# Kernel tuning notes

Hardware: AMD Instinct MI355X
Metric: run time of the kernel (lower is better)

The kernel has to match this reference:

```python
import jax, jax.numpy as jnp
import numpy as np

N_NODES = 100000
N_EDGES = 300000
F = 256


def setup_inputs() -> dict:
    key = jax.random.key(0)
    k1, k2, k3, k4, k5, k6 = jax.random.split(key, 6)
    x = jax.random.normal(k1, (N_NODES, F), dtype=jnp.float32)
    edge_index = jax.random.randint(k2, (2, N_EDGES), 0, N_NODES, dtype=jnp.int32)
    # GCNConv learned params (PyG: lin weight [out,in] applied as x @ W.T; store as [in,out])
    W_conv = jax.random.normal(k3, (F, F), dtype=jnp.float32) / np.sqrt(F)
    b_conv = jax.random.normal(k4, (F,), dtype=jnp.float32) * 0.01
    W_lin = jax.random.normal(k5, (F, 1), dtype=jnp.float32) / np.sqrt(F)
    b_lin = jax.random.normal(k6, (1,), dtype=jnp.float32) * 0.01
    return {"x": x, "edge_index": edge_index, "W_conv": W_conv,
            "b_conv": b_conv, "W_lin": W_lin, "b_lin": b_lin}


def gcn_conv(x, edge_index, W_conv, b_conv):
    N = x.shape[0]
    # add self loops (PyG default add_self_loops=True)
    loop = jnp.arange(N, dtype=edge_index.dtype)
    src = jnp.concatenate([edge_index[0], loop])
    dst = jnp.concatenate([edge_index[1], loop])
    # symmetric normalization: deg over destination, norm = d^-1/2[src]*d^-1/2[dst]
    deg = jax.ops.segment_sum(jnp.ones_like(dst, dtype=x.dtype), dst, num_segments=N)
    dinv = jnp.where(deg > 0, jax.lax.rsqrt(deg), 0.0)
    norm = dinv[src] * dinv[dst]  # [E+N]
    h = x @ W_conv  # [N,F] dense transform first (PyG order)
    msg = h[src] * norm[:, None]  # gather + scale, [E+N, F]
    agg = jax.ops.segment_sum(msg, dst, num_segments=N)  # scatter-add, [N,F]
    return agg + b_conv


def reference(x, edge_index, W_conv, b_conv, W_lin, b_lin):
    h = jax.nn.relu(gcn_conv(x, edge_index, W_conv, b_conv))
    return jax.nn.sigmoid(h @ W_lin + b_lin)  # [N,1]
```

## Files before the change

kernel.cpp:

```cpp
#include <hip/hip_runtime.h>
#include <hip/hip_bf16.h>
#include <math.h>

#define FDIM 256

typedef short bfrag __attribute__((ext_vector_type(8)));
typedef short s16x4 __attribute__((ext_vector_type(4)));
typedef float f32x4 __attribute__((ext_vector_type(4)));
typedef unsigned short u16x8 __attribute__((ext_vector_type(8)));

__device__ __forceinline__ short f2bf_rne(float f) {
    uint32_t u = __float_as_uint(f);
    uint32_t r = (u + 0x7FFFu + ((u >> 16) & 1u)) >> 16;
    return (short)r;
}
__device__ __forceinline__ float bf2f(unsigned short s) {
    return __uint_as_float(((uint32_t)s) << 16);
}

#define GLOAD_LDS16(g, l) __builtin_amdgcn_global_load_lds(              \
    (const __attribute__((address_space(1))) void*)(g),                  \
    (__attribute__((address_space(3))) void*)(l), 16, 0, 0)

__global__ void count_kernel(const int* __restrict__ dst, int* __restrict__ counts, int E) {
    int e = blockIdx.x * 256 + threadIdx.x;
    if (e < E) atomicAdd(&counts[dst[e]], 1);
}

__global__ void scan1_kernel(const int* __restrict__ counts, int* __restrict__ blksums, int N) {
    __shared__ int sd[256];
    int tid = threadIdx.x;
    int base = blockIdx.x * 1024 + tid * 4;
    int s = 0;
#pragma unroll
    for (int t = 0; t < 4; ++t) { int i = base + t; if (i < N) s += counts[i]; }
    sd[tid] = s; __syncthreads();
    for (int off = 128; off > 0; off >>= 1) {
        if (tid < off) sd[tid] += sd[tid + off];
        __syncthreads();
    }
    if (tid == 0) blksums[blockIdx.x] = sd[0];
}

__global__ void scan2_kernel(int* __restrict__ blksums, int NB) {
    __shared__ int sd[128];
    int tid = threadIdx.x;
    int v = (tid < NB) ? blksums[tid] : 0;
    sd[tid] = v; __syncthreads();
    for (int off = 1; off < 128; off <<= 1) {
        int t = (tid >= off) ? sd[tid - off] : 0;
        __syncthreads();
        sd[tid] += t;
        __syncthreads();
    }
    if (tid < NB) blksums[tid] = sd[tid] - v;
}

__global__ void scan3_kernel(const int* __restrict__ counts, const int* __restrict__ blksums,
                             int* __restrict__ offsets, int* __restrict__ cursor,
                             float* __restrict__ dinv, int N, int E) {
    __shared__ int sd[256];
    int tid = threadIdx.x;
    int base = blockIdx.x * 1024 + tid * 4;
    int c[4]; int s = 0;
#pragma unroll
    for (int t = 0; t < 4; ++t) { int i = base + t; c[t] = (i < N) ? counts[i] : 0; s += c[t]; }
    sd[tid] = s; __syncthreads();
    int v = s;
    for (int off = 1; off < 256; off <<= 1) {
        int t = (tid >= off) ? sd[tid - off] : 0;
        __syncthreads();
        sd[tid] += t;
        __syncthreads();
    }
    int run = sd[tid] - v + blksums[blockIdx.x];
#pragma unroll
    for (int t = 0; t < 4; ++t) {
        int i = base + t;
        if (i < N) {
            offsets[i] = run;
            cursor[i]  = run;
            dinv[i] = rsqrtf((float)(c[t] + 1));
            run += c[t];
        }
    }
    if (blockIdx.x == 0 && tid == 0) offsets[N] = E;
}

__global__ void fill_kernel(const int* __restrict__ src, const int* __restrict__ dst,
                            int* __restrict__ cursor, int* __restrict__ csr_src, int E) {
    int e = blockIdx.x * 256 + threadIdx.x;
    if (e < E) {
        int s = src[e], d = dst[e];
        int pos = atomicAdd(&cursor[d], 1);
        csr_src[pos] = s;
    }
}

__global__ void wsplit_kernel(const float* __restrict__ W,
                              short* __restrict__ Wh, short* __restrict__ Wl) {
    const int k = blockIdx.x;
    const int n = threadIdx.x;
    const float w = W[k * 256 + n];
    const short hi = f2bf_rne(w);
    const short lo = f2bf_rne(w - bf2f((unsigned short)hi));
    const int s = k >> 5, g = (k & 31) >> 3, j = k & 7;
    const size_t idx = (size_t)s * 8192 + n * 32 + g * 8 + j;
    Wh[idx] = hi; Wl[idx] = lo;
}

__global__ __launch_bounds__(512, 4) void gemm_mfma(const float* __restrict__ X,
                                                    const short* __restrict__ Wth,
                                                    const short* __restrict__ Wtl,
                                                    const float* __restrict__ dinv,
                                                    unsigned short* __restrict__ Hb, int N) {
    __shared__ short Xh[2][2048], Xl[2][2048];
    __shared__ short Wh[2][8192], Wl[2][8192];

    const int tid  = threadIdx.x;
    const int lane = tid & 63;
    const int wid  = tid >> 6;
    const int wm   = wid >> 2;
    const int wn   = wid & 3;
    const int row0 = blockIdx.x * 64;
    const int g    = lane >> 4;
    const int r15  = lane & 15;

    const int srow = tid >> 3, skq = tid & 7;
    const int sg = skq >> 1, sj = (skq & 1) * 4;
    const int xoff = (srow * 4 + sg) * 8 + sj;
    const int xrow = row0 + srow;
    const float* xptr = X + (size_t)xrow * FDIM + skq * 4;

    f32x4 acc[2][4];
#pragma unroll
    for (int i = 0; i < 2; ++i)
#pragma unroll
        for (int j = 0; j < 4; ++j) acc[i][j] = (f32x4){0.f, 0.f, 0.f, 0.f};

    float4 xa;
    xa = (xrow < N) ? *(const float4*)xptr : make_float4(0, 0, 0, 0);
    {
        const float v[4] = {xa.x, xa.y, xa.z, xa.w};
        s16x4 hi4, lo4;
#pragma unroll
        for (int j = 0; j < 4; ++j) {
            const short h = f2bf_rne(v[j]);
            hi4[j] = h; lo4[j] = f2bf_rne(v[j] - bf2f((unsigned short)h));
        }
        *(s16x4*)(&Xh[0][xoff]) = hi4;
        *(s16x4*)(&Xl[0][xoff]) = lo4;
    }
#pragma unroll
    for (int p = 0; p < 2; ++p) {
        GLOAD_LDS16(Wth + p * 4096 + tid * 8, &Wh[0][p * 4096 + tid * 8]);
        GLOAD_LDS16(Wtl + p * 4096 + tid * 8, &Wl[0][p * 4096 + tid * 8]);
    }
    xa = (xrow < N) ? *(const float4*)(xptr + 32) : make_float4(0, 0, 0, 0);
    __syncthreads();

    for (int s = 0; s < 8; ++s) {
        const int cur = s & 1, nxt = cur ^ 1;
        if (s < 7) {
            const float v[4] = {xa.x, xa.y, xa.z, xa.w};
            s16x4 hi4, lo4;
#pragma unroll
            for (int j = 0; j < 4; ++j) {
                const short h = f2bf_rne(v[j]);
                hi4[j] = h; lo4[j] = f2bf_rne(v[j] - bf2f((unsigned short)h));
            }
            *(s16x4*)(&Xh[nxt][xoff]) = hi4;
            *(s16x4*)(&Xl[nxt][xoff]) = lo4;
            const short* gh = Wth + (s + 1) * 8192;
            const short* gl = Wtl + (s + 1) * 8192;
#pragma unroll
            for (int p = 0; p < 2; ++p) {
                GLOAD_LDS16(gh + p * 4096 + tid * 8, &Wh[nxt][p * 4096 + tid * 8]);
                GLOAD_LDS16(gl + p * 4096 + tid * 8, &Wl[nxt][p * 4096 + tid * 8]);
            }
        }
        if (s < 6)
            xa = (xrow < N) ? *(const float4*)(xptr + (s + 2) * 32) : make_float4(0, 0, 0, 0);

        bfrag ah[2], al[2], bh[4], bl[4];
#pragma unroll
        for (int mi = 0; mi < 2; ++mi) {
            const int off = ((wm * 32 + mi * 16 + r15) * 4 + g) * 8;
            ah[mi] = *(const bfrag*)(&Xh[cur][off]);
            al[mi] = *(const bfrag*)(&Xl[cur][off]);
        }
#pragma unroll
        for (int ni = 0; ni < 4; ++ni) {
            const int off = ((wn * 64 + ni * 16 + r15) * 4 + g) * 8;
            bh[ni] = *(const bfrag*)(&Wh[cur][off]);
            bl[ni] = *(const bfrag*)(&Wl[cur][off]);
        }
#pragma unroll
        for (int mi = 0; mi < 2; ++mi)
#pragma unroll
            for (int ni = 0; ni < 4; ++ni)
                acc[mi][ni] = __builtin_amdgcn_mfma_f32_16x16x32_bf16(ah[mi], bh[ni], acc[mi][ni], 0, 0, 0);
#pragma unroll
        for (int mi = 0; mi < 2; ++mi)
#pragma unroll
            for (int ni = 0; ni < 4; ++ni)
                acc[mi][ni] = __builtin_amdgcn_mfma_f32_16x16x32_bf16(ah[mi], bl[ni], acc[mi][ni], 0, 0, 0);
#pragma unroll
        for (int mi = 0; mi < 2; ++mi)
#pragma unroll
            for (int ni = 0; ni < 4; ++ni)
                acc[mi][ni] = __builtin_amdgcn_mfma_f32_16x16x32_bf16(al[mi], bh[ni], acc[mi][ni], 0, 0, 0);

        if (s < 7) __syncthreads();
    }

#pragma unroll
    for (int mi = 0; mi < 2; ++mi) {
        const int rowb = row0 + wm * 32 + mi * 16 + g * 4;
#pragma unroll
        for (int r = 0; r < 4; ++r) {
            const int row = rowb + r;
            if (row < N) {
                const float dv = dinv[row];
                unsigned short* base = Hb + (size_t)row * FDIM + wn * 64 + r15;
#pragma unroll
                for (int ni = 0; ni < 4; ++ni)
                    base[ni * 16] = (unsigned short)f2bf_rne(acc[mi][ni][r] * dv);
            }
        }
    }
}

__global__ __launch_bounds__(256) void agg_kernel(const unsigned short* __restrict__ hb,
                                                  const int* __restrict__ offsets,
                                                  const int* __restrict__ csr_src,
                                                  const float* __restrict__ dinv,
                                                  const float* __restrict__ b_conv,
                                                  const float* __restrict__ W_lin,
                                                  const float* __restrict__ b_lin,
                                                  float* __restrict__ out, int N) {
    const int t    = threadIdx.x;
    const int l16  = t & 15;
    const int node = blockIdx.x * 16 + (t >> 4);
    if (node >= N) return;

    const int start = offsets[node];
    const int end   = offsets[node + 1];

    float acc[16];
    {
        const unsigned short* r = hb + (size_t)node * FDIM + l16 * 16;
        const u16x8 u0 = *(const u16x8*)r, u1 = *(const u16x8*)(r + 8);
#pragma unroll
        for (int k = 0; k < 8; ++k) { acc[k] = bf2f(u0[k]); acc[8 + k] = bf2f(u1[k]); }
    }
    for (int j = start; j < end; ++j) {
        const unsigned short* r = hb + (size_t)csr_src[j] * FDIM + l16 * 16;
        const u16x8 u0 = *(const u16x8*)r, u1 = *(const u16x8*)(r + 8);
#pragma unroll
        for (int k = 0; k < 8; ++k) { acc[k] += bf2f(u0[k]); acc[8 + k] += bf2f(u1[k]); }
    }

    const float dv = dinv[node];
    float p = 0.f;
#pragma unroll
    for (int q = 0; q < 4; ++q) {
        const float4 bc = *(const float4*)(b_conv + l16 * 16 + q * 4);
        const float4 wl = *(const float4*)(W_lin  + l16 * 16 + q * 4);
        p = fmaf(fmaxf(fmaf(acc[q * 4 + 0], dv, bc.x), 0.f), wl.x, p);
        p = fmaf(fmaxf(fmaf(acc[q * 4 + 1], dv, bc.y), 0.f), wl.y, p);
        p = fmaf(fmaxf(fmaf(acc[q * 4 + 2], dv, bc.z), 0.f), wl.z, p);
        p = fmaf(fmaxf(fmaf(acc[q * 4 + 3], dv, bc.w), 0.f), wl.w, p);
    }
#pragma unroll
    for (int off = 1; off < 16; off <<= 1) p += __shfl_xor(p, off);
    if (l16 == 0) out[node] = 1.f / (1.f + expf(-(p + b_lin[0])));
}

extern "C" void kernel_launch(void* const* d_in, const int* in_sizes, int n_in,
                              void* d_out, int out_size, void* d_ws, size_t ws_size,
                              hipStream_t stream) {
    const float* x      = (const float*)d_in[0];
    const int*   eidx   = (const int*)d_in[1];
    const float* W_conv = (const float*)d_in[2];
    const float* b_conv = (const float*)d_in[3];
    const float* W_lin  = (const float*)d_in[4];
    const float* b_lin  = (const float*)d_in[5];
    float* out = (float*)d_out;

    const int N = in_sizes[0] / FDIM;
    const int E = in_sizes[1] / 2;
    const int* e_src = eidx;
    const int* e_dst = eidx + E;

    char* p = (char*)d_ws;
    unsigned short* hb = (unsigned short*)p; p += (size_t)N * FDIM * sizeof(unsigned short);
    int* counts   = (int*)p;        p += (size_t)N * sizeof(int);
    int* offsets  = (int*)p;        p += (size_t)(N + 1) * sizeof(int);
    int* cursor   = (int*)p;        p += (size_t)N * sizeof(int);
    float* dinv   = (float*)p;      p += (size_t)N * sizeof(float);
    int* csr_src  = (int*)p;        p += (size_t)E * sizeof(int);
    int* blksums  = (int*)p;        p += 128 * sizeof(int);
    short* Wth    = (short*)p;      p += (size_t)FDIM * FDIM * sizeof(short);
    short* Wtl    = (short*)p;      p += (size_t)FDIM * FDIM * sizeof(short);

    const int NB = (N + 1023) / 1024;

    hipMemsetAsync(counts, 0, (size_t)N * sizeof(int), stream);

    count_kernel<<<(E + 255) / 256, 256, 0, stream>>>(e_dst, counts, E);
    scan1_kernel<<<NB, 256, 0, stream>>>(counts, blksums, N);
    scan2_kernel<<<1, 128, 0, stream>>>(blksums, NB);
    scan3_kernel<<<NB, 256, 0, stream>>>(counts, blksums, offsets, cursor, dinv, N, E);
    fill_kernel<<<(E + 255) / 256, 256, 0, stream>>>(e_src, e_dst, cursor, csr_src, E);

    wsplit_kernel<<<FDIM, FDIM, 0, stream>>>(W_conv, Wth, Wtl);

    gemm_mfma<<<(N + 63) / 64, 512, 0, stream>>>(x, Wth, Wtl, dinv, hb, N);

    agg_kernel<<<(N + 15) / 16, 256, 0, stream>>>(hb, offsets, csr_src, dinv,
                                                  b_conv, W_lin, b_lin, out, N);
}
```

Measured before the change: 269.2 us.

## Load W fragments directly to registers in GEMM and unroll edge gather by two

The GEMM no longer stages the split-bf16 W tiles through LDS with global_load_lds. Each wave now loads its B fragments straight from global memory (cache-resident) into double-buffered registers one k-step ahead. The X LDS tile is relaid out as k-group-major to change its bank access pattern, and the k-loop is fully unrolled. The aggregation kernel processes two neighbours per iteration with two accumulator sets to expose more memory-level parallelism, at the cost of more registers, which may reduce occupancy.

```diff
diff --git a/kernel.cpp b/kernel.cpp
--- a/kernel.cpp
+++ b/kernel.cpp
@@ -17,10 +17,6 @@
 __device__ __forceinline__ float bf2f(unsigned short s) {
     return __uint_as_float(((uint32_t)s) << 16);
 }
-
-#define GLOAD_LDS16(g, l) __builtin_amdgcn_global_load_lds(              \
-    (const __attribute__((address_space(1))) void*)(g),                  \
-    (__attribute__((address_space(3))) void*)(l), 16, 0, 0)
 
 __global__ void count_kernel(const int* __restrict__ dst, int* __restrict__ counts, int E) {
     int e = blockIdx.x * 256 + threadIdx.x;
@@ -115,7 +111,6 @@
                                                     const float* __restrict__ dinv,
                                                     unsigned short* __restrict__ Hb, int N) {
     __shared__ short Xh[2][2048], Xl[2][2048];
-    __shared__ short Wh[2][8192], Wl[2][8192];
 
     const int tid  = threadIdx.x;
     const int lane = tid & 63;
@@ -126,9 +121,11 @@
     const int g    = lane >> 4;
     const int r15  = lane & 15;
 
+    const short* WhP = Wth + (wn * 64 + r15) * 32 + g * 8;
+    const short* WlP = Wtl + (wn * 64 + r15) * 32 + g * 8;
+
     const int srow = tid >> 3, skq = tid & 7;
-    const int sg = skq >> 1, sj = (skq & 1) * 4;
-    const int xoff = (srow * 4 + sg) * 8 + sj;
+    const int xsidx = (skq >> 1) * 512 + srow * 8 + (skq & 1) * 4;
     const int xrow = row0 + srow;
     const float* xptr = X + (size_t)xrow * FDIM + skq * 4;
 
@@ -138,8 +135,9 @@
 #pragma unroll
         for (int j = 0; j < 4; ++j) acc[i][j] = (f32x4){0.f, 0.f, 0.f, 0.f};
 
-    float4 xa;
-    xa = (xrow < N) ? *(const float4*)xptr : make_float4(0, 0, 0, 0);
+    bfrag bh[2][4], bl[2][4];
+
+    float4 xa = (xrow < N) ? *(const float4*)xptr : make_float4(0, 0, 0, 0);
     {
         const float v[4] = {xa.x, xa.y, xa.z, xa.w};
         s16x4 hi4, lo4;
@@ -148,19 +146,21 @@
             const short h = f2bf_rne(v[j]);
             hi4[j] = h; lo4[j] = f2bf_rne(v[j] - bf2f((unsigned short)h));
         }
-        *(s16x4*)(&Xh[0][xoff]) = hi4;
-        *(s16x4*)(&Xl[0][xoff]) = lo4;
-    }
-#pragma unroll
-    for (int p = 0; p < 2; ++p) {
-        GLOAD_LDS16(Wth + p * 4096 + tid * 8, &Wh[0][p * 4096 + tid * 8]);
-        GLOAD_LDS16(Wtl + p * 4096 + tid * 8, &Wl[0][p * 4096 + tid * 8]);
+        *(s16x4*)(&Xh[0][xsidx]) = hi4;
+        *(s16x4*)(&Xl[0][xsidx]) = lo4;
+    }
+#pragma unroll
+    for (int ni = 0; ni < 4; ++ni) {
+        bh[0][ni] = *(const bfrag*)(WhP + ni * 512);
+        bl[0][ni] = *(const bfrag*)(WlP + ni * 512);
     }
     xa = (xrow < N) ? *(const float4*)(xptr + 32) : make_float4(0, 0, 0, 0);
     __syncthreads();
 
+#pragma unroll
     for (int s = 0; s < 8; ++s) {
         const int cur = s & 1, nxt = cur ^ 1;
+
         if (s < 7) {
             const float v[4] = {xa.x, xa.y, xa.z, xa.w};
             s16x4 hi4, lo4;
@@ -169,47 +169,43 @@
                 const short h = f2bf_rne(v[j]);
                 hi4[j] = h; lo4[j] = f2bf_rne(v[j] - bf2f((unsigned short)h));
             }
-            *(s16x4*)(&Xh[nxt][xoff]) = hi4;
-            *(s16x4*)(&Xl[nxt][xoff]) = lo4;
-            const short* gh = Wth + (s + 1) * 8192;
-            const short* gl = Wtl + (s + 1) * 8192;
-#pragma unroll
-            for (int p = 0; p < 2; ++p) {
-                GLOAD_LDS16(gh + p * 4096 + tid * 8, &Wh[nxt][p * 4096 + tid * 8]);
-                GLOAD_LDS16(gl + p * 4096 + tid * 8, &Wl[nxt][p * 4096 + tid * 8]);
-            }
+            *(s16x4*)(&Xh[nxt][xsidx]) = hi4;
+            *(s16x4*)(&Xl[nxt][xsidx]) = lo4;
         }
         if (s < 6)
             xa = (xrow < N) ? *(const float4*)(xptr + (s + 2) * 32) : make_float4(0, 0, 0, 0);
 
-        bfrag ah[2], al[2], bh[4], bl[4];
+        if (s < 7) {
+#pragma unroll
+            for (int ni = 0; ni < 4; ++ni) {
+                bh[nxt][ni] = *(const bfrag*)(WhP + (s + 1) * 8192 + ni * 512);
+                bl[nxt][ni] = *(const bfrag*)(WlP + (s + 1) * 8192 + ni * 512);
+            }
+        }
+
+        bfrag ah[2], al[2];
 #pragma unroll
         for (int mi = 0; mi < 2; ++mi) {
-            const int off = ((wm * 32 + mi * 16 + r15) * 4 + g) * 8;
+            const int off = g * 512 + (wm * 32 + mi * 16 + r15) * 8;
             ah[mi] = *(const bfrag*)(&Xh[cur][off]);
             al[mi] = *(const bfrag*)(&Xl[cur][off]);
         }
-#pragma unroll
-        for (int ni = 0; ni < 4; ++ni) {
-            const int off = ((wn * 64 + ni * 16 + r15) * 4 + g) * 8;
-            bh[ni] = *(const bfrag*)(&Wh[cur][off]);
-            bl[ni] = *(const bfrag*)(&Wl[cur][off]);
-        }
+
 #pragma unroll
         for (int mi = 0; mi < 2; ++mi)
 #pragma unroll
             for (int ni = 0; ni < 4; ++ni)
-                acc[mi][ni] = __builtin_amdgcn_mfma_f32_16x16x32_bf16(ah[mi], bh[ni], acc[mi][ni], 0, 0, 0);
+                acc[mi][ni] = __builtin_amdgcn_mfma_f32_16x16x32_bf16(ah[mi], bh[cur][ni], acc[mi][ni], 0, 0, 0);
 #pragma unroll
         for (int mi = 0; mi < 2; ++mi)
 #pragma unroll
             for (int ni = 0; ni < 4; ++ni)
-                acc[mi][ni] = __builtin_amdgcn_mfma_f32_16x16x32_bf16(ah[mi], bl[ni], acc[mi][ni], 0, 0, 0);
+                acc[mi][ni] = __builtin_amdgcn_mfma_f32_16x16x32_bf16(ah[mi], bl[cur][ni], acc[mi][ni], 0, 0, 0);
 #pragma unroll
         for (int mi = 0; mi < 2; ++mi)
 #pragma unroll
             for (int ni = 0; ni < 4; ++ni)
-                acc[mi][ni] = __builtin_amdgcn_mfma_f32_16x16x32_bf16(al[mi], bh[ni], acc[mi][ni], 0, 0, 0);
+                acc[mi][ni] = __builtin_amdgcn_mfma_f32_16x16x32_bf16(al[mi], bh[cur][ni], acc[mi][ni], 0, 0, 0);
 
         if (s < 7) __syncthreads();
     }
@@ -247,18 +243,33 @@
     const int start = offsets[node];
     const int end   = offsets[node + 1];
 
-    float acc[16];
+    float accA[16], accB[16];
     {
         const unsigned short* r = hb + (size_t)node * FDIM + l16 * 16;
         const u16x8 u0 = *(const u16x8*)r, u1 = *(const u16x8*)(r + 8);
 #pragma unroll
-        for (int k = 0; k < 8; ++k) { acc[k] = bf2f(u0[k]); acc[8 + k] = bf2f(u1[k]); }
-    }
-    for (int j = start; j < end; ++j) {
-        const unsigned short* r = hb + (size_t)csr_src[j] * FDIM + l16 * 16;
-        const u16x8 u0 = *(const u16x8*)r, u1 = *(const u16x8*)(r + 8);
-#pragma unroll
-        for (int k = 0; k < 8; ++k) { acc[k] += bf2f(u0[k]); acc[8 + k] += bf2f(u1[k]); }
+        for (int k = 0; k < 8; ++k) {
+            accA[k] = bf2f(u0[k]); accA[8 + k] = bf2f(u1[k]);
+            accB[k] = 0.f;         accB[8 + k] = 0.f;
+        }
+    }
+    int j = start;
+    for (; j + 1 < end; j += 2) {
+        const unsigned short* ra = hb + (size_t)csr_src[j]     * FDIM + l16 * 16;
+        const unsigned short* rb = hb + (size_t)csr_src[j + 1] * FDIM + l16 * 16;
+        const u16x8 a0 = *(const u16x8*)ra, a1 = *(const u16x8*)(ra + 8);
+        const u16x8 b0 = *(const u16x8*)rb, b1 = *(const u16x8*)(rb + 8);
+#pragma unroll
+        for (int k = 0; k < 8; ++k) {
+            accA[k] += bf2f(a0[k]); accA[8 + k] += bf2f(a1[k]);
+            accB[k] += bf2f(b0[k]); accB[8 + k] += bf2f(b1[k]);
+        }
+    }
+    if (j < end) {
+        const unsigned short* ra = hb + (size_t)csr_src[j] * FDIM + l16 * 16;
+        const u16x8 a0 = *(const u16x8*)ra, a1 = *(const u16x8*)(ra + 8);
+#pragma unroll
+        for (int k = 0; k < 8; ++k) { accA[k] += bf2f(a0[k]); accA[8 + k] += bf2f(a1[k]); }
     }
 
     const float dv = dinv[node];
@@ -267,10 +278,10 @@
     for (int q = 0; q < 4; ++q) {
         const float4 bc = *(const float4*)(b_conv + l16 * 16 + q * 4);
         const float4 wl = *(const float4*)(W_lin  + l16 * 16 + q * 4);
-        p = fmaf(fmaxf(fmaf(acc[q * 4 + 0], dv, bc.x), 0.f), wl.x, p);
-        p = fmaf(fmaxf(fmaf(acc[q * 4 + 1], dv, bc.y), 0.f), wl.y, p);
-        p = fmaf(fmaxf(fmaf(acc[q * 4 + 2], dv, bc.z), 0.f), wl.z, p);
-        p = fmaf(fmaxf(fmaf(acc[q * 4 + 3], dv, bc.w), 0.f), wl.w, p);
+        p = fmaf(fmaxf(fmaf(accA[q * 4 + 0] + accB[q * 4 + 0], dv, bc.x), 0.f), wl.x, p);
+        p = fmaf(fmaxf(fmaf(accA[q * 4 + 1] + accB[q * 4 + 1], dv, bc.y), 0.f), wl.y, p);
+        p = fmaf(fmaxf(fmaf(accA[q * 4 + 2] + accB[q * 4 + 2], dv, bc.z), 0.f), wl.z, p);
+        p = fmaf(fmaxf(fmaf(accA[q * 4 + 3] + accB[q * 4 + 3], dv, bc.w), 0.f), wl.w, p);
     }
 #pragma unroll
     for (int off = 1; off < 16; off <<= 1) p += __shfl_xor(p, off);
```

Result: slower. 291.8 us (+8.4%).

## Enlarge GEMM row tile, swizzle W LDS layout, batch neighbor gathers in aggregation

Applied to the files above, without the earlier changes.

The GEMM block now covers 128 rows instead of 64, so each wave holds 4x4 MFMA tiles. This reuses each W fragment across more rows and halves the number of blocks that reload W. The W layout in LDS is XOR-swizzled and X is stored in a k-group-major layout, both meant to reduce LDS bank conflicts on fragment reads. The aggregation kernel preloads up to 16 neighbor indices per node into lanes, broadcasts them with shuffles, and issues four row gathers at once to expose memory-level parallelism. The trade-off is higher register and LDS use per GEMM block, which lowers occupancy (launch bounds go from 4 to 2).

```diff
diff --git a/kernel.cpp b/kernel.cpp
--- a/kernel.cpp
+++ b/kernel.cpp
@@ -5,7 +5,6 @@
 #define FDIM 256
 
 typedef short bfrag __attribute__((ext_vector_type(8)));
-typedef short s16x4 __attribute__((ext_vector_type(4)));
 typedef float f32x4 __attribute__((ext_vector_type(4)));
 typedef unsigned short u16x8 __attribute__((ext_vector_type(8)));
 
@@ -105,16 +104,16 @@
     const short hi = f2bf_rne(w);
     const short lo = f2bf_rne(w - bf2f((unsigned short)hi));
     const int s = k >> 5, g = (k & 31) >> 3, j = k & 7;
-    const size_t idx = (size_t)s * 8192 + n * 32 + g * 8 + j;
+    const size_t idx = (size_t)s * 8192 + ((n * 32 + g * 8) ^ ((n & 7) << 3)) + j;
     Wh[idx] = hi; Wl[idx] = lo;
 }
 
-__global__ __launch_bounds__(512, 4) void gemm_mfma(const float* __restrict__ X,
+__global__ __launch_bounds__(512, 2) void gemm_mfma(const float* __restrict__ X,
                                                     const short* __restrict__ Wth,
                                                     const short* __restrict__ Wtl,
                                                     const float* __restrict__ dinv,
                                                     unsigned short* __restrict__ Hb, int N) {
-    __shared__ short Xh[2][2048], Xl[2][2048];
+    __shared__ short Xh[2][4096], Xl[2][4096];
     __shared__ short Wh[2][8192], Wl[2][8192];
 
     const int tid  = threadIdx.x;
@@ -122,55 +121,59 @@
     const int wid  = tid >> 6;
     const int wm   = wid >> 2;
     const int wn   = wid & 3;
-    const int row0 = blockIdx.x * 64;
+    const int row0 = blockIdx.x * 128;
     const int g    = lane >> 4;
     const int r15  = lane & 15;
-
-    const int srow = tid >> 3, skq = tid & 7;
-    const int sg = skq >> 1, sj = (skq & 1) * 4;
-    const int xoff = (srow * 4 + sg) * 8 + sj;
+    const int bswz = (r15 & 7) << 3;
+
+    const int srow = tid >> 2, sc = tid & 3;
+    const int xsidx = sc * 1024 + srow * 8;
     const int xrow = row0 + srow;
-    const float* xptr = X + (size_t)xrow * FDIM + skq * 4;
-
-    f32x4 acc[2][4];
-#pragma unroll
-    for (int i = 0; i < 2; ++i)
+    const float* xptr = X + (size_t)xrow * FDIM + 8 * sc;
+
+    f32x4 acc[4][4];
+#pragma unroll
+    for (int i = 0; i < 4; ++i)
 #pragma unroll
         for (int j = 0; j < 4; ++j) acc[i][j] = (f32x4){0.f, 0.f, 0.f, 0.f};
 
-    float4 xa;
-    xa = (xrow < N) ? *(const float4*)xptr : make_float4(0, 0, 0, 0);
+    float4 xa0, xa1;
+    if (xrow < N) { xa0 = *(const float4*)xptr; xa1 = *(const float4*)(xptr + 4); }
+    else          { xa0 = make_float4(0,0,0,0); xa1 = make_float4(0,0,0,0); }
     {
-        const float v[4] = {xa.x, xa.y, xa.z, xa.w};
-        s16x4 hi4, lo4;
-#pragma unroll
-        for (int j = 0; j < 4; ++j) {
+        const float v[8] = {xa0.x,xa0.y,xa0.z,xa0.w,xa1.x,xa1.y,xa1.z,xa1.w};
+        bfrag hi8, lo8;
+#pragma unroll
+        for (int j = 0; j < 8; ++j) {
             const short h = f2bf_rne(v[j]);
-            hi4[j] = h; lo4[j] = f2bf_rne(v[j] - bf2f((unsigned short)h));
-        }
-        *(s16x4*)(&Xh[0][xoff]) = hi4;
-        *(s16x4*)(&Xl[0][xoff]) = lo4;
+            hi8[j] = h; lo8[j] = f2bf_rne(v[j] - bf2f((unsigned short)h));
+        }
+        *(bfrag*)(&Xh[0][xsidx]) = hi8;
+        *(bfrag*)(&Xl[0][xsidx]) = lo8;
     }
 #pragma unroll
     for (int p = 0; p < 2; ++p) {
         GLOAD_LDS16(Wth + p * 4096 + tid * 8, &Wh[0][p * 4096 + tid * 8]);
         GLOAD_LDS16(Wtl + p * 4096 + tid * 8, &Wl[0][p * 4096 + tid * 8]);
     }
-    xa = (xrow < N) ? *(const float4*)(xptr + 32) : make_float4(0, 0, 0, 0);
+    if (xrow < N) { xa0 = *(const float4*)(xptr + 32); xa1 = *(const float4*)(xptr + 36); }
+    else          { xa0 = make_float4(0,0,0,0); xa1 = make_float4(0,0,0,0); }
     __syncthreads();
 
+#pragma unroll
     for (int s = 0; s < 8; ++s) {
         const int cur = s & 1, nxt = cur ^ 1;
+
         if (s < 7) {
-            const float v[4] = {xa.x, xa.y, xa.z, xa.w};
-            s16x4 hi4, lo4;
-#pragma unroll
-            for (int j = 0; j < 4; ++j) {
+            const float v[8] = {xa0.x,xa0.y,xa0.z,xa0.w,xa1.x,xa1.y,xa1.z,xa1.w};
+            bfrag hi8, lo8;
+#pragma unroll
+            for (int j = 0; j < 8; ++j) {
                 const short h = f2bf_rne(v[j]);
-                hi4[j] = h; lo4[j] = f2bf_rne(v[j] - bf2f((unsigned short)h));
+                hi8[j] = h; lo8[j] = f2bf_rne(v[j] - bf2f((unsigned short)h));
             }
-            *(s16x4*)(&Xh[nxt][xoff]) = hi4;
-            *(s16x4*)(&Xl[nxt][xoff]) = lo4;
+            *(bfrag*)(&Xh[nxt][xsidx]) = hi8;
+            *(bfrag*)(&Xl[nxt][xsidx]) = lo8;
             const short* gh = Wth + (s + 1) * 8192;
             const short* gl = Wtl + (s + 1) * 8192;
 #pragma unroll
@@ -179,34 +182,39 @@
                 GLOAD_LDS16(gl + p * 4096 + tid * 8, &Wl[nxt][p * 4096 + tid * 8]);
             }
         }
-        if (s < 6)
-            xa = (xrow < N) ? *(const float4*)(xptr + (s + 2) * 32) : make_float4(0, 0, 0, 0);
-
-        bfrag ah[2], al[2], bh[4], bl[4];
-#pragma unroll
-        for (int mi = 0; mi < 2; ++mi) {
-            const int off = ((wm * 32 + mi * 16 + r15) * 4 + g) * 8;
+        if (s < 6) {
+            if (xrow < N) {
+                const float* src = xptr + (s + 2) * 32;
+                xa0 = *(const float4*)src; xa1 = *(const float4*)(src + 4);
+            } else { xa0 = make_float4(0,0,0,0); xa1 = make_float4(0,0,0,0); }
+        }
+
+        bfrag ah[4], al[4], bh[4], bl[4];
+#pragma unroll
+        for (int mi = 0; mi < 4; ++mi) {
+            const int off = g * 1024 + (wm * 64 + mi * 16 + r15) * 8;
             ah[mi] = *(const bfrag*)(&Xh[cur][off]);
             al[mi] = *(const bfrag*)(&Xl[cur][off]);
         }
 #pragma unroll
         for (int ni = 0; ni < 4; ++ni) {
-            const int off = ((wn * 64 + ni * 16 + r15) * 4 + g) * 8;
+            const int off = (((wn * 64 + ni * 16 + r15) * 32 + g * 8) ^ bswz);
             bh[ni] = *(const bfrag*)(&Wh[cur][off]);
             bl[ni] = *(const bfrag*)(&Wl[cur][off]);
         }
-#pragma unroll
-        for (int mi = 0; mi < 2; ++mi)
+
+#pragma unroll
+        for (int mi = 0; mi < 4; ++mi)
 #pragma unroll
             for (int ni = 0; ni < 4; ++ni)
                 acc[mi][ni] = __builtin_amdgcn_mfma_f32_16x16x32_bf16(ah[mi], bh[ni], acc[mi][ni], 0, 0, 0);
 #pragma unroll
-        for (int mi = 0; mi < 2; ++mi)
+        for (int mi = 0; mi < 4; ++mi)
 #pragma unroll
             for (int ni = 0; ni < 4; ++ni)
                 acc[mi][ni] = __builtin_amdgcn_mfma_f32_16x16x32_bf16(ah[mi], bl[ni], acc[mi][ni], 0, 0, 0);
 #pragma unroll
-        for (int mi = 0; mi < 2; ++mi)
+        for (int mi = 0; mi < 4; ++mi)
 #pragma unroll
             for (int ni = 0; ni < 4; ++ni)
                 acc[mi][ni] = __builtin_amdgcn_mfma_f32_16x16x32_bf16(al[mi], bh[ni], acc[mi][ni], 0, 0, 0);
@@ -215,8 +223,8 @@
     }
 
 #pragma unroll
-    for (int mi = 0; mi < 2; ++mi) {
-        const int rowb = row0 + wm * 32 + mi * 16 + g * 4;
+    for (int mi = 0; mi < 4; ++mi) {
+        const int rowb = row0 + wm * 64 + mi * 16 + g * 4;
 #pragma unroll
         for (int r = 0; r < 4; ++r) {
             const int row = rowb + r;
@@ -246,6 +254,9 @@
 
     const int start = offsets[node];
     const int end   = offsets[node + 1];
+    const int deg   = end - start;
+
+    int idx16 = (l16 < deg) ? csr_src[start + l16] : 0;
 
     float acc[16];
     {
@@ -254,11 +265,40 @@
 #pragma unroll
         for (int k = 0; k < 8; ++k) { acc[k] = bf2f(u0[k]); acc[8 + k] = bf2f(u1[k]); }
     }
-    for (int j = start; j < end; ++j) {
+
+    const int dcap = deg < 16 ? deg : 16;
+    int k = 0;
+    for (; k + 4 <= dcap; k += 4) {
+        const int s0 = __shfl(idx16, k,     16);
+        const int s1 = __shfl(idx16, k + 1, 16);
+        const int s2 = __shfl(idx16, k + 2, 16);
+        const int s3 = __shfl(idx16, k + 3, 16);
+        const unsigned short* r0 = hb + (size_t)s0 * FDIM + l16 * 16;
+        const unsigned short* r1 = hb + (size_t)s1 * FDIM + l16 * 16;
+        const unsigned short* r2 = hb + (size_t)s2 * FDIM + l16 * 16;
+        const unsigned short* r3 = hb + (size_t)s3 * FDIM + l16 * 16;
+        const u16x8 a0 = *(const u16x8*)r0, a1 = *(const u16x8*)(r0 + 8);
+        const u16x8 b0 = *(const u16x8*)r1, b1 = *(const u16x8*)(r1 + 8);
+        const u16x8 c0 = *(const u16x8*)r2, c1 = *(const u16x8*)(r2 + 8);
+        const u16x8 d0 = *(const u16x8*)r3, d1 = *(const u16x8*)(r3 + 8);
+#pragma unroll
+        for (int q = 0; q < 8; ++q) {
+            acc[q]     += (bf2f(a0[q]) + bf2f(b0[q])) + (bf2f(c0[q]) + bf2f(d0[q]));
+            acc[8 + q] += (bf2f(a1[q]) + bf2f(b1[q])) + (bf2f(c1[q]) + bf2f(d1[q]));
+        }
+    }
+    for (; k < dcap; ++k) {
+        const int s0 = __shfl(idx16, k, 16);
+        const unsigned short* r = hb + (size_t)s0 * FDIM + l16 * 16;
+        const u16x8 u0 = *(const u16x8*)r, u1 = *(const u16x8*)(r + 8);
+#pragma unroll
+        for (int q = 0; q < 8; ++q) { acc[q] += bf2f(u0[q]); acc[8 + q] += bf2f(u1[q]); }
+    }
+    for (int j = start + 16; j < end; ++j) {
         const unsigned short* r = hb + (size_t)csr_src[j] * FDIM + l16 * 16;
         const u16x8 u0 = *(const u16x8*)r, u1 = *(const u16x8*)(r + 8);
 #pragma unroll
-        for (int k = 0; k < 8; ++k) { acc[k] += bf2f(u0[k]); acc[8 + k] += bf2f(u1[k]); }
+        for (int q = 0; q < 8; ++q) { acc[q] += bf2f(u0[q]); acc[8 + q] += bf2f(u1[q]); }
     }
 
     const float dv = dinv[node];
@@ -316,7 +356,7 @@
 
     wsplit_kernel<<<FDIM, FDIM, 0, stream>>>(W_conv, Wth, Wtl);
 
-    gemm_mfma<<<(N + 63) / 64, 512, 0, stream>>>(x, Wth, Wtl, dinv, hb, N);
+    gemm_mfma<<<(N + 127) / 128, 512, 0, stream>>>(x, Wth, Wtl, dinv, hb, N);
 
     agg_kernel<<<(N + 15) / 16, 256, 0, stream>>>(hb, offsets, csr_src, dinv,
                                                   b_conv, W_lin, b_lin, out, N);
```

After: 277.7 us. +3.2%, slower.
